# Kernel tuning notes

Hardware: AMD Instinct MI355X
Metric: run time of the kernel (lower is better)

## Reference

```python
import jax, jax.numpy as jnp
import numpy as np

INPUT_SIZE = 512
HIDDEN = 1024
OUT = 4
SEQ = 2048


def setup_inputs() -> dict:
    key = jax.random.key(0)
    ks = jax.random.split(key, 12)
    s_in = 1.0 / np.sqrt(INPUT_SIZE)
    s_h = 1.0 / np.sqrt(HIDDEN)
    inp = {
        "x": jax.random.normal(ks[0], (SEQ, INPUT_SIZE), jnp.float32),
        "h0": jnp.zeros((1, 1, HIDDEN), jnp.float32),
        "c0": jnp.zeros((1, 1, HIDDEN), jnp.float32),
        # LSTM params (PyTorch layout: gates ordered i, f, g, o along 4H)
        "w_ih": jax.random.uniform(ks[1], (4 * HIDDEN, INPUT_SIZE), jnp.float32, -s_h, s_h),
        "w_hh": jax.random.uniform(ks[2], (4 * HIDDEN, HIDDEN), jnp.float32, -s_h, s_h),
        "b_ih": jax.random.uniform(ks[3], (4 * HIDDEN,), jnp.float32, -s_h, s_h),
        "b_hh": jax.random.uniform(ks[4], (4 * HIDDEN,), jnp.float32, -s_h, s_h),
        "fc1_w": jax.random.uniform(ks[5], (HIDDEN, HIDDEN), jnp.float32, -s_h, s_h),
        "fc1_b": jax.random.uniform(ks[6], (HIDDEN,), jnp.float32, -s_h, s_h),
        "fc2_w": jax.random.uniform(ks[7], (HIDDEN, HIDDEN), jnp.float32, -s_h, s_h),
        "fc2_b": jax.random.uniform(ks[8], (HIDDEN,), jnp.float32, -s_h, s_h),
        "mean_w": jax.random.uniform(ks[9], (OUT, HIDDEN), jnp.float32, -s_h, s_h),
        "mean_b": jax.random.uniform(ks[10], (OUT,), jnp.float32, -s_h, s_h),
        "log_std": jnp.zeros((OUT,), jnp.float32),
    }
    return inp


def _lstm(x, h0, c0, w_ih, w_hh, b_ih, b_hh):
    # Precompute input projections for all timesteps: [T, 4H]
    gx = x @ w_ih.T + b_ih + b_hh
    H = h0.shape[-1]

    def step(carry, gx_t):
        h, c = carry  # [H], [H]
        g = gx_t + h @ w_hh.T  # [4H]
        i = jax.nn.sigmoid(g[0 * H:1 * H])
        f = jax.nn.sigmoid(g[1 * H:2 * H])
        gg = jnp.tanh(g[2 * H:3 * H])
        o = jax.nn.sigmoid(g[3 * H:4 * H])
        c_new = f * c + i * gg
        h_new = o * jnp.tanh(c_new)
        return (h_new, c_new), h_new

    (hT, cT), ys = jax.lax.scan(step, (h0[0, 0], c0[0, 0]), gx)
    return ys, hT[None, None, :], cT[None, None, :]  # ys: [T, H]


def reference(x, h0, c0, w_ih, w_hh, b_ih, b_hh, fc1_w, fc1_b, fc2_w, fc2_b, mean_w, mean_b, log_std):
    ys, hT, cT = _lstm(x, h0, c0, w_ih, w_hh, b_ih, b_hh)
    h1 = jax.nn.relu(ys @ fc1_w.T + fc1_b)
    h2 = jax.nn.relu(h1 @ fc2_w.T + fc2_b)
    action_mean = h2 @ mean_w.T + mean_b  # [T, OUT]
    action_log_std = jnp.broadcast_to(log_std, action_mean.shape)
    return action_mean, action_log_std, hT, cT
```

## Files before the change

### kernel.cpp

```cpp
#include <hip/hip_runtime.h>
#include <stdint.h>


#define T_SEQ 2048
#define H 1024
#define G4 4096
#define K_IN 512
#define SENT 0x7FC0DEADu

__device__ __forceinline__ float sigmoidf_(float x) { return 1.0f / (1.0f + __expf(-x)); }
__device__ __forceinline__ float tanhf_(float x) { return 1.0f - 2.0f / (1.0f + __expf(2.0f * x)); }

__device__ __forceinline__ uint4 poll_load16(const uint4* p) {
  uint4 v;
  asm volatile("global_load_dwordx4 %0, %1, off sc0 sc1\n\ts_waitcnt vmcnt(0)"
               : "=v"(v) : "v"(p) : "memory");
  return v;
}

__global__ void init_k(const float* __restrict__ h0, float* __restrict__ h_hist) {
  int idx = blockIdx.x * blockDim.x + threadIdx.x;
  if (idx < H) {
    h_hist[idx] = h0[idx];
  } else if (idx < (T_SEQ + 1) * H) {
    ((unsigned*)h_hist)[idx] = SENT;
  }
}

#define BM 64
#define BN 64
#define BK 32
#define LDT 68

template <bool RELU, bool HASB2>
__global__ __launch_bounds__(256) void gemm_bias_k(
    const float* __restrict__ A, const float* __restrict__ Bw,
    const float* __restrict__ b1, const float* __restrict__ b2,
    float* __restrict__ C, int M, int N, int K) {
  __shared__ float As[BK][LDT];
  __shared__ float Bs[BK][LDT];
  const int tid = threadIdx.x;
  const int m0 = blockIdx.y * BM;
  const int n0 = blockIdx.x * BN;
  const int tx = tid & 15, ty = tid >> 4;
  const int srow = tid >> 2;
  const int skq = tid & 3;

  float acc[4][4];
#pragma unroll
  for (int i = 0; i < 4; i++)
#pragma unroll
    for (int j = 0; j < 4; j++) acc[i][j] = 0.f;

  const float* Arow = A + (size_t)(m0 + srow) * K;
  const float* Brow = Bw + (size_t)(n0 + srow) * K;

  for (int k0 = 0; k0 < K; k0 += BK) {
    float4 a0 = *(const float4*)(Arow + k0 + skq * 8);
    float4 a1 = *(const float4*)(Arow + k0 + skq * 8 + 4);
    float4 c0_ = *(const float4*)(Brow + k0 + skq * 8);
    float4 c1_ = *(const float4*)(Brow + k0 + skq * 8 + 4);
    __syncthreads();
    const int kb = skq * 8;
    As[kb + 0][srow] = a0.x; As[kb + 1][srow] = a0.y; As[kb + 2][srow] = a0.z; As[kb + 3][srow] = a0.w;
    As[kb + 4][srow] = a1.x; As[kb + 5][srow] = a1.y; As[kb + 6][srow] = a1.z; As[kb + 7][srow] = a1.w;
    Bs[kb + 0][srow] = c0_.x; Bs[kb + 1][srow] = c0_.y; Bs[kb + 2][srow] = c0_.z; Bs[kb + 3][srow] = c0_.w;
    Bs[kb + 4][srow] = c1_.x; Bs[kb + 5][srow] = c1_.y; Bs[kb + 6][srow] = c1_.z; Bs[kb + 7][srow] = c1_.w;
    __syncthreads();
#pragma unroll
    for (int kk = 0; kk < BK; kk++) {
      float av[4], bv[4];
      *(float4*)av = *(const float4*)&As[kk][ty * 4];
      *(float4*)bv = *(const float4*)&Bs[kk][tx * 4];
#pragma unroll
      for (int i = 0; i < 4; i++)
#pragma unroll
        for (int j = 0; j < 4; j++) acc[i][j] = fmaf(av[i], bv[j], acc[i][j]);
    }
  }

  float bb[4];
#pragma unroll
  for (int j = 0; j < 4; j++) {
    bb[j] = b1[n0 + tx * 4 + j];
    if (HASB2) bb[j] += b2[n0 + tx * 4 + j];
  }
#pragma unroll
  for (int i = 0; i < 4; i++) {
    float4 o;
    float* op = (float*)&o;
#pragma unroll
    for (int j = 0; j < 4; j++) {
      float v = acc[i][j] + bb[j];
      op[j] = RELU ? fmaxf(v, 0.f) : v;
    }
    *(float4*)&C[(size_t)(m0 + ty * 4 + i) * N + n0 + tx * 4] = o;
  }
}

#define NWG 128
#define NTHR 512
#define HPAD 68

#define PIN4(V) asm volatile("" : "+v"((V).x), "+v"((V).y), "+v"((V).z), "+v"((V).w))

__global__ __attribute__((amdgpu_waves_per_eu(2, 2))) __launch_bounds__(NTHR)
void lstm_k(
    const float* __restrict__ gx, const float* __restrict__ w_hh,
    const float* __restrict__ c0, float* __restrict__ h_hist,
    float* __restrict__ out) {
  unsigned* h_u = (unsigned*)h_hist;
  __shared__ float hbuf[2][16 * HPAD];
  const int tid = threadIdx.x;
  const int wg = blockIdx.x;
  const int wave = tid >> 6, lane = tid & 63;
  const int g = lane & 3;
  const int s = lane >> 2;
  const int unit = wg * 8 + wave;
  const int grow = g * 1024 + unit;

  const float* wp = w_hh + (size_t)grow * H + s * 64;
  float4 w0 = *(const float4*)(wp + 0),  w1 = *(const float4*)(wp + 4);
  float4 w2 = *(const float4*)(wp + 8),  w3 = *(const float4*)(wp + 12);
  float4 w4 = *(const float4*)(wp + 16), w5 = *(const float4*)(wp + 20);
  float4 w6 = *(const float4*)(wp + 24), w7 = *(const float4*)(wp + 28);
  float4 w8 = *(const float4*)(wp + 32), w9 = *(const float4*)(wp + 36);
  float4 wA = *(const float4*)(wp + 40), wB = *(const float4*)(wp + 44);
  float4 wC = *(const float4*)(wp + 48), wD = *(const float4*)(wp + 52);
  float4 wE = *(const float4*)(wp + 56), wF = *(const float4*)(wp + 60);
  PIN4(w0); PIN4(w1); PIN4(w2); PIN4(w3);
  PIN4(w4); PIN4(w5); PIN4(w6); PIN4(w7);
  PIN4(w8); PIN4(w9); PIN4(wA); PIN4(wB);
  PIN4(wC); PIN4(wD); PIN4(wE); PIN4(wF);

  float c = c0[unit];

  const bool poller = tid < 256;
  const int stage_idx = 4 * tid + (tid >> 4) * 4;

  for (int t = 0; t < T_SEQ; t++) {
    const int buf = t & 1;
    float gxv = gx[(size_t)t * G4 + grow];
    asm volatile("" : "+v"(gxv));

    if (poller) {
      const uint4* src = (const uint4*)(h_u + (size_t)t * H) + tid;
      uint4 v = poll_load16(src);
      while (v.x == SENT || v.y == SENT || v.z == SENT || v.w == SENT) {
        __builtin_amdgcn_s_sleep(1);
        v = poll_load16(src);
      }
      float4 f;
      f.x = __uint_as_float(v.x); f.y = __uint_as_float(v.y);
      f.z = __uint_as_float(v.z); f.w = __uint_as_float(v.w);
      *(float4*)&hbuf[buf][stage_idx] = f;
    }
    __syncthreads();

    float acc0 = 0.f, acc1 = 0.f, acc2 = 0.f, acc3 = 0.f;
    const float* hs = &hbuf[buf][s * HPAD];
#define MAC(J, WV)                                  \
  {                                                 \
    float4 hv = *(const float4*)(hs + (J) * 4);     \
    acc0 = fmaf((WV).x, hv.x, acc0);                \
    acc1 = fmaf((WV).y, hv.y, acc1);                \
    acc2 = fmaf((WV).z, hv.z, acc2);                \
    acc3 = fmaf((WV).w, hv.w, acc3);                \
  }
    MAC(0, w0) MAC(1, w1) MAC(2, w2) MAC(3, w3)
    MAC(4, w4) MAC(5, w5) MAC(6, w6) MAC(7, w7)
    MAC(8, w8) MAC(9, w9) MAC(10, wA) MAC(11, wB)
    MAC(12, wC) MAC(13, wD) MAC(14, wE) MAC(15, wF)
#undef MAC
    float accv = (acc0 + acc1) + (acc2 + acc3);
    accv += __shfl_xor(accv, 4);
    accv += __shfl_xor(accv, 8);
    accv += __shfl_xor(accv, 16);
    accv += __shfl_xor(accv, 32);
    float pre = accv + gxv;
    float act = (g == 2) ? tanhf_(pre) : sigmoidf_(pre);
    float b1v = __shfl_xor(act, 1);
    float b2v = __shfl_xor(act, 2);
    float b3v = __shfl_xor(act, 3);
    c = fmaf(b1v, c, act * b2v);
    float hn = b3v * tanhf_(c);
    if (lane == 0) {
      __hip_atomic_store(&h_u[(size_t)(t + 1) * H + unit], __float_as_uint(hn),
                         __ATOMIC_RELAXED, __HIP_MEMORY_SCOPE_AGENT);
      if (t == T_SEQ - 1) {
        out[16384 + unit] = hn;
        out[17408 + unit] = c;
      }
    }
  }
}

__global__ __launch_bounds__(256) void head_k(
    const float* __restrict__ h2, const float* __restrict__ mean_w,
    const float* __restrict__ mean_b, const float* __restrict__ log_std,
    float* __restrict__ out) {
  const int t = blockIdx.x;
  const int tid = threadIdx.x;
  const int wave = tid >> 6, lane = tid & 63;
  const float* hr = h2 + (size_t)t * H;
  const float* wr = mean_w + (size_t)wave * H;
  float s = 0.f;
#pragma unroll
  for (int j = 0; j < 16; j++) s = fmaf(hr[lane + j * 64], wr[lane + j * 64], s);
#pragma unroll
  for (int off = 32; off > 0; off >>= 1) s += __shfl_down(s, off);
  if (lane == 0) out[t * 4 + wave] = s + mean_b[wave];
  if (tid < 4) out[8192 + t * 4 + tid] = log_std[tid];
}

extern "C" void kernel_launch(void* const* d_in, const int* in_sizes, int n_in,
                              void* d_out, int out_size, void* d_ws, size_t ws_size,
                              hipStream_t stream) {
  const float* x      = (const float*)d_in[0];
  const float* h0     = (const float*)d_in[1];
  const float* c0     = (const float*)d_in[2];
  const float* w_ih   = (const float*)d_in[3];
  const float* w_hh   = (const float*)d_in[4];
  const float* b_ih   = (const float*)d_in[5];
  const float* b_hh   = (const float*)d_in[6];
  const float* fc1_w  = (const float*)d_in[7];
  const float* fc1_b  = (const float*)d_in[8];
  const float* fc2_w  = (const float*)d_in[9];
  const float* fc2_b  = (const float*)d_in[10];
  const float* mean_w = (const float*)d_in[11];
  const float* mean_b = (const float*)d_in[12];
  const float* lstd   = (const float*)d_in[13];
  float* out = (float*)d_out;

  float* gx = (float*)d_ws;
  float* h_hist = gx + (size_t)T_SEQ * G4;
  float* h1 = gx;
  float* h2 = gx + (size_t)T_SEQ * H;

  init_k<<<dim3((T_SEQ + 1) * H / 256), 256, 0, stream>>>(h0, h_hist);
  gemm_bias_k<false, true><<<dim3(G4 / BN, T_SEQ / BM), 256, 0, stream>>>(
      x, w_ih, b_ih, b_hh, gx, T_SEQ, G4, K_IN);
  lstm_k<<<dim3(NWG), NTHR, 0, stream>>>(gx, w_hh, c0, h_hist, out);
  gemm_bias_k<true, false><<<dim3(H / BN, T_SEQ / BM), 256, 0, stream>>>(
      h_hist + H, fc1_w, fc1_b, nullptr, h1, T_SEQ, H, H);
  gemm_bias_k<true, false><<<dim3(H / BN, T_SEQ / BM), 256, 0, stream>>>(
      h1, fc2_w, fc2_b, nullptr, h2, T_SEQ, H, H);
  head_k<<<dim3(T_SEQ), 256, 0, stream>>>(h2, mean_w, mean_b, lstd, out);
}
```

Before: 3.978 ms.

## Relay per-step hidden state through per-XCD L2 mirror with tag polling

Each XCD elects one leader workgroup by ticket. The leader polls the global h history with cache-bypassing loads and copies each step into a per-XCD ring mirror, then publishes a tag. Other workgroups on that XCD poll the tag with sc0 loads, which can hit in the shared L2, and read the mirror instead of hammering system-coherent memory, falling back to the global array every few spins. This is meant to cut cross-die polling traffic and latency on the recurrent step barrier. In exchange it adds a relay hop through the leader, and it relies on XCC_ID mapping and on the L2 coherence of the ring buffer being correct.

```diff
diff --git a/kernel.cpp b/kernel.cpp
--- a/kernel.cpp
+++ b/kernel.cpp
@@ -7,6 +7,9 @@
 #define G4 4096
 #define K_IN 512
 #define SENT 0x7FC0DEADu
+#define RSTRIDE ((T_SEQ + 1) * H)
+#define RING 8
+#define NXCD 8
 
 __device__ __forceinline__ float sigmoidf_(float x) { return 1.0f / (1.0f + __expf(-x)); }
 __device__ __forceinline__ float tanhf_(float x) { return 1.0f - 2.0f / (1.0f + __expf(2.0f * x)); }
@@ -17,14 +20,41 @@
                : "=v"(v) : "v"(p) : "memory");
   return v;
 }
+__device__ __forceinline__ unsigned poll_load4_sc0(const unsigned* p) {
+  unsigned v;
+  asm volatile("global_load_dword %0, %1, off sc0\n\ts_waitcnt vmcnt(0)"
+               : "=v"(v) : "v"(p) : "memory");
+  return v;
+}
+__device__ __forceinline__ uint4 load16_sc0(const uint4* p) {
+  uint4 v;
+  asm volatile("global_load_dwordx4 %0, %1, off sc0\n\ts_waitcnt vmcnt(0)"
+               : "=v"(v) : "v"(p) : "memory");
+  return v;
+}
+__device__ __forceinline__ int get_xcc() {
+  int x;
+  asm("s_getreg_b32 %0, hwreg(HW_REG_XCC_ID, 0, 4)" : "=s"(x));
+  return x & (NXCD - 1);
+}
+__device__ __forceinline__ bool has_sent(uint4 v) {
+  unsigned m = v.x ^ SENT;
+  m = min(m, v.y ^ SENT); m = min(m, v.z ^ SENT); m = min(m, v.w ^ SENT);
+  return m == 0;
+}
 
 __global__ void init_k(const float* __restrict__ h0, float* __restrict__ h_hist) {
   int idx = blockIdx.x * blockDim.x + threadIdx.x;
   if (idx < H) {
     h_hist[idx] = h0[idx];
-  } else if (idx < (T_SEQ + 1) * H) {
+  } else if (idx < RSTRIDE) {
     ((unsigned*)h_hist)[idx] = SENT;
   }
+}
+__global__ void init2_k(unsigned* __restrict__ tags, unsigned* __restrict__ tickets) {
+  int idx = threadIdx.x;
+  if (idx < NXCD * RING) tags[idx] = 0;
+  if (idx < NXCD) tickets[idx] = 0;
 }
 
 #define BM 64
@@ -108,9 +138,11 @@
 void lstm_k(
     const float* __restrict__ gx, const float* __restrict__ w_hh,
     const float* __restrict__ c0, float* __restrict__ h_hist,
-    float* __restrict__ out) {
+    unsigned* __restrict__ mirror, unsigned* __restrict__ tags,
+    unsigned* __restrict__ tickets, float* __restrict__ out) {
   unsigned* h_u = (unsigned*)h_hist;
   __shared__ float hbuf[2][16 * HPAD];
+  __shared__ int sh_xcc, sh_dual;
   const int tid = threadIdx.x;
   const int wg = blockIdx.x;
   const int wave = tid >> 6, lane = tid & 63;
@@ -135,20 +167,48 @@
 
   float c = c0[unit];
 
+  if (tid == 0) {
+    int x = get_xcc();
+    sh_xcc = x;
+    sh_dual = (atomicAdd(&tickets[x], 1u) == 0u) ? 1 : 0;
+  }
+  __syncthreads();
+  const int xcc = sh_xcc;
+  const bool dual = sh_dual != 0;
+  unsigned* mir = mirror + (size_t)xcc * RING * H;
+  unsigned* tg = tags + (size_t)xcc * RING;
+
   const bool poller = tid < 256;
   const int stage_idx = 4 * tid + (tid >> 4) * 4;
 
   for (int t = 0; t < T_SEQ; t++) {
     const int buf = t & 1;
+    const int slot = t & (RING - 1);
     float gxv = gx[(size_t)t * G4 + grow];
     asm volatile("" : "+v"(gxv));
 
     if (poller) {
-      const uint4* src = (const uint4*)(h_u + (size_t)t * H) + tid;
-      uint4 v = poll_load16(src);
-      while (v.x == SENT || v.y == SENT || v.z == SENT || v.w == SENT) {
-        __builtin_amdgcn_s_sleep(1);
-        v = poll_load16(src);
+      uint4 v;
+      if (dual) {
+        const uint4* srcg = (const uint4*)(h_u + (size_t)t * H) + tid;
+        v = poll_load16(srcg);
+        while (has_sent(v)) v = poll_load16(srcg);
+        ((uint4*)(mir + (size_t)slot * H))[tid] = v;
+        asm volatile("s_waitcnt vmcnt(0)" ::: "memory");
+      } else {
+        const uint4* srcm = (const uint4*)(mir + (size_t)slot * H) + tid;
+        const uint4* srcg = (const uint4*)(h_u + (size_t)t * H) + tid;
+        const int want = t + 1;
+        int spins = 0;
+        for (;;) {
+          unsigned tv = poll_load4_sc0(&tg[slot]);
+          if ((int)tv >= want) { v = load16_sc0(srcm); break; }
+          if (++spins == 6) {
+            spins = 0;
+            uint4 d = poll_load16(srcg);
+            if (!has_sent(d)) { v = d; break; }
+          }
+        }
       }
       float4 f;
       f.x = __uint_as_float(v.x); f.y = __uint_as_float(v.y);
@@ -156,6 +216,7 @@
       *(float4*)&hbuf[buf][stage_idx] = f;
     }
     __syncthreads();
+    if (dual && tid == 0) ((volatile unsigned*)tg)[slot] = (unsigned)(t + 1);
 
     float acc0 = 0.f, acc1 = 0.f, acc2 = 0.f, acc3 = 0.f;
     const float* hs = &hbuf[buf][s * HPAD];
@@ -184,7 +245,7 @@
     float b3v = __shfl_xor(act, 3);
     c = fmaf(b1v, c, act * b2v);
     float hn = b3v * tanhf_(c);
-    if (lane == 0) {
+    if (g == 0 && s == 0) {
       __hip_atomic_store(&h_u[(size_t)(t + 1) * H + unit], __float_as_uint(hn),
                          __ATOMIC_RELAXED, __HIP_MEMORY_SCOPE_AGENT);
       if (t == T_SEQ - 1) {
@@ -234,13 +295,18 @@
 
   float* gx = (float*)d_ws;
   float* h_hist = gx + (size_t)T_SEQ * G4;
+  unsigned* mirror = (unsigned*)(h_hist + RSTRIDE);
+  unsigned* tags = mirror + (size_t)NXCD * RING * H;
+  unsigned* tickets = tags + NXCD * RING;
   float* h1 = gx;
   float* h2 = gx + (size_t)T_SEQ * H;
 
-  init_k<<<dim3((T_SEQ + 1) * H / 256), 256, 0, stream>>>(h0, h_hist);
+  init_k<<<dim3((RSTRIDE + 255) / 256), 256, 0, stream>>>(h0, h_hist);
+  init2_k<<<dim3(1), 256, 0, stream>>>(tags, tickets);
   gemm_bias_k<false, true><<<dim3(G4 / BN, T_SEQ / BM), 256, 0, stream>>>(
       x, w_ih, b_ih, b_hh, gx, T_SEQ, G4, K_IN);
-  lstm_k<<<dim3(NWG), NTHR, 0, stream>>>(gx, w_hh, c0, h_hist, out);
+  lstm_k<<<dim3(NWG), NTHR, 0, stream>>>(gx, w_hh, c0, h_hist, mirror, tags,
+                                         tickets, out);
   gemm_bias_k<true, false><<<dim3(H / BN, T_SEQ / BM), 256, 0, stream>>>(
       h_hist + H, fc1_w, fc1_b, nullptr, h1, T_SEQ, H, H);
   gemm_bias_k<true, false><<<dim3(H / BN, T_SEQ / BM), 256, 0, stream>>>(
```

Result: slower. 6.279 ms (+57.8%).
